# Kernel tuning notes

Measured on AMD Instinct MI355X. Metric: run time of the kernel, lower is better.

The kernel has to match this reference:

```python
import jax, jax.numpy as jnp
import numpy as np
from jax import lax

DIM = 256
WS = 8            # window side -> N = 64
H = 8             # num_heads
HD = DIM // H     # head dim = 32
NREF = 30
RB = 4            # reference batch
NWIN = 144        # windows per image (96x96 / 8x8)
N = WS * WS
B_ = RB * NWIN
SCALE = HD ** -0.5
LN_EPS = 1e-5


def make_rel_index():
    coords = np.stack(np.meshgrid(np.arange(WS), np.arange(WS), indexing='ij'))  # (2,WS,WS)
    cf = coords.reshape(2, -1)
    rel = (cf[:, :, None] - cf[:, None, :]).transpose(1, 2, 0).astype(np.int64)
    rel[..., 0] += WS - 1
    rel[..., 1] += WS - 1
    rel[..., 0] *= 2 * WS - 1
    return jnp.asarray(rel.sum(-1), jnp.int32)  # (N, N)


def setup_inputs() -> dict:
    key = jax.random.key(0)
    ks = jax.random.split(key, 10)
    return {
        'x': jax.random.normal(ks[0], (B_, N, DIM), jnp.float32),
        'mask': jnp.zeros((NWIN, N, N), jnp.float32),
        'x_ref': jax.random.normal(ks[1], (RB, DIM, NREF), jnp.float32),
        'qkv_w': jax.random.normal(ks[2], (3 * DIM, DIM), jnp.float32) * 0.02,
        'qkv_b': jnp.zeros((3 * DIM,), jnp.float32),
        'proj_w': jax.random.normal(ks[3], (DIM, DIM), jnp.float32) * 0.02,
        'proj_b': jnp.zeros((DIM,), jnp.float32),
        'bias_table': jax.random.normal(ks[4], ((2 * WS - 1) ** 2, H), jnp.float32) * 0.02,
        'diff_mu': jax.random.normal(ks[5], (1, 1, DIM), jnp.float32),
        'diff_logsigma': jax.random.normal(ks[6], (1, 1, DIM), jnp.float32) * 0.05,
        'ref_qk_w': jax.random.normal(ks[7], (2 * NREF, NREF), jnp.float32) * 0.1,
        'ref_qk_b': jnp.zeros((2 * NREF,), jnp.float32),
        'conv_w': jax.random.normal(ks[8], (H, H, 3, 3), jnp.float32) * 0.05,
        'conv_b': jnp.zeros((H,), jnp.float32),
        'rel_index': make_rel_index(),
    }


def _layer_norm_2d(a):
    # layer norm over the last two dims, no affine (F.layer_norm(x, [n_win*N, n_rf]))
    m = jnp.mean(a, axis=(-2, -1), keepdims=True)
    v = jnp.var(a, axis=(-2, -1), keepdims=True)
    return (a - m) * lax.rsqrt(v + LN_EPS)


def reference(x, mask, x_ref, qkv_w, qkv_b, proj_w, proj_b, bias_table,
              diff_mu, diff_logsigma, ref_qk_w, ref_qk_b, conv_w, conv_b, rel_index):
    # qkv projection -> (3, B_, H, N, HD)
    qkv = (x @ qkv_w.T + qkv_b).reshape(B_, N, 3, H, HD).transpose(2, 0, 3, 1, 4)
    q, k, v = qkv[0], qkv[1], qkv[2]

    # reference queries/values: x_ref (RB, DIM, NREF) -> (RB, 2*NREF, DIM)
    ref = (x_ref @ ref_qk_w.T + ref_qk_b).transpose(0, 2, 1)
    ref_q = diff_mu + jnp.exp(diff_logsigma) * ref[:, :NREF]   # (RB, NREF, DIM)
    ref_q = ref_q.reshape(RB, NREF, H, HD).transpose(0, 2, 1, 3)       # (RB, H, NREF, HD)
    ref_v = ref[:, NREF:].reshape(RB, NREF, H, HD).transpose(0, 2, 1, 3)

    # cross-attn scores q @ ref_k^T, broadcast ref over windows of the same batch
    qb = q.reshape(RB, NWIN, H, N, HD)
    ref_attn = jnp.einsum('bwhnd,bhrd->bhwnr', qb, ref_q)  # (RB, H, NWIN, N, NREF)
    ref_attn = ref_attn.reshape(RB, H, NWIN * N, NREF)

    # 3-step conv diffusion refinement with layernorm+gelu residual
    for _ in range(3):
        upd = lax.conv_general_dilated(
            ref_attn, conv_w, window_strides=(1, 1), padding=((1, 1), (1, 1)),
            dimension_numbers=('NCHW', 'OIHW', 'NCHW')) + conv_b[None, :, None, None]
        ref_attn = ref_attn + jax.nn.gelu(_layer_norm_2d(upd), approximate=False)

    ref_attn = ref_attn.reshape(RB, H, NWIN, N, NREF).transpose(0, 2, 1, 3, 4)  # (RB,NWIN,H,N,NREF)
    ref_attn = jax.nn.softmax(ref_attn, axis=-1)
    q_new = jnp.einsum('bwhnr,bhrd->bwhnd', ref_attn, ref_v) * SCALE

    # window attention with relative position bias + mask
    attn = jnp.einsum('bwhnd,bwhmd->bwhnm', q_new, k.reshape(RB, NWIN, H, N, HD))
    rel_bias = bias_table[rel_index.reshape(-1)].reshape(N, N, H).transpose(2, 0, 1)  # (H,N,N)
    attn = attn + rel_bias[None, None] + mask[None, :, None]
    attn = jax.nn.softmax(attn, axis=-1)

    out = jnp.einsum('bwhnm,bwhmd->bwhnd', attn, v.reshape(RB, NWIN, H, N, HD))
    out = out.transpose(0, 1, 3, 2, 4).reshape(B_, N, DIM)
    return out @ proj_w.T + proj_b
```

## Files before the change

### kernel.cpp

```cpp
#include <hip/hip_runtime.h>
#include <math.h>

#define NHD 8
#define HD 32
#define NREF 30
#define RB 4
#define NWIN 144
#define NTOK 64
#define IMG_H (NWIN*NTOK)
#define LN_CNT (IMG_H*NREF)
#define SCALE 0.1767766952966369f
#define LN_EPS 1e-5f

typedef __attribute__((ext_vector_type(8))) short bf8_t;
typedef __attribute__((ext_vector_type(4))) float f4_t;

__device__ __forceinline__ float gelu_f(float v) {
    return 0.5f * v * (1.0f + erff(v * 0.7071067811865476f));
}

__device__ __forceinline__ short f2bf(float f) {
    union { float f; unsigned u; } v; v.f = f;
    unsigned r = v.u + 0x7fffu + ((v.u >> 16) & 1u);
    return (short)(r >> 16);
}

__device__ __forceinline__ float bf2f(unsigned short u) {
    union { unsigned u; float f; } v; v.u = ((unsigned)u) << 16;
    return v.f;
}

__global__ __launch_bounds__(256) void k_prep(
    const float* __restrict__ x, unsigned short* __restrict__ xb,
    const float* __restrict__ qkv_w, unsigned short* __restrict__ wqb,
    const float* __restrict__ proj_w, unsigned short* __restrict__ wpb,
    const float* __restrict__ mask, const float* __restrict__ bias_table,
    const int* __restrict__ rel_index, float* __restrict__ bmt,
    const float* __restrict__ x_ref, const float* __restrict__ rw,
    const float* __restrict__ rbias, const float* __restrict__ dmu,
    const float* __restrict__ dls, float* __restrict__ ref_q,
    float* __restrict__ ref_v) {
    __shared__ float shbuf[4160 + 1800];
    const int bid = blockIdx.x;
    const int t = threadIdx.x;
    if (bid < 2048) {
        const int n8 = 9437184 / 8;
        for (int i = bid * 256 + t; i < n8; i += 2048 * 256) {
            const float* s = x + (size_t)i * 8;
            float4 a = *reinterpret_cast<const float4*>(s);
            float4 b = *reinterpret_cast<const float4*>(s + 4);
            bf8_t p;
            p[0] = f2bf(a.x); p[1] = f2bf(a.y); p[2] = f2bf(a.z); p[3] = f2bf(a.w);
            p[4] = f2bf(b.x); p[5] = f2bf(b.y); p[6] = f2bf(b.z); p[7] = f2bf(b.w);
            *reinterpret_cast<bf8_t*>(xb + (size_t)i * 8) = p;
        }
    } else if (bid < 2192) {
        const int w = bid - 2048;
        float* lm = shbuf;
        float* lb = shbuf + 4160;
        for (int u = t; u < 4096; u += 256)
            lm[(u >> 6) * 65 + (u & 63)] = mask[(size_t)w * 4096 + u];
        for (int u = t; u < 1800; u += 256) lb[u] = bias_table[u];
        __syncthreads();
        for (int u = t; u < 4096; u += 256) {
            const int m = u >> 6, n = u & 63;
            const float mv = lm[n * 65 + m];
            const int ri = rel_index[n * 64 + m];
#pragma unroll
            for (int h = 0; h < 8; ++h)
                bmt[(size_t)(w * 8 + h) * 4096 + u] = mv + lb[ri * 8 + h];
        }
    } else if (bid < 2288) {
        const int b2 = bid - 2192;
        const int n8 = 196608 / 8;
        for (int i = b2 * 256 + t; i < n8; i += 96 * 256) {
            const float* s = qkv_w + (size_t)i * 8;
            float4 a = *reinterpret_cast<const float4*>(s);
            float4 b = *reinterpret_cast<const float4*>(s + 4);
            bf8_t p;
            p[0] = f2bf(a.x); p[1] = f2bf(a.y); p[2] = f2bf(a.z); p[3] = f2bf(a.w);
            p[4] = f2bf(b.x); p[5] = f2bf(b.y); p[6] = f2bf(b.z); p[7] = f2bf(b.w);
            *reinterpret_cast<bf8_t*>(wqb + (size_t)i * 8) = p;
        }
    } else if (bid < 2320) {
        const int b2 = bid - 2288;
        const int n8 = 65536 / 8;
        for (int i = b2 * 256 + t; i < n8; i += 32 * 256) {
            const float* s = proj_w + (size_t)i * 8;
            float4 a = *reinterpret_cast<const float4*>(s);
            float4 b = *reinterpret_cast<const float4*>(s + 4);
            bf8_t p;
            p[0] = f2bf(a.x); p[1] = f2bf(a.y); p[2] = f2bf(a.z); p[3] = f2bf(a.w);
            p[4] = f2bf(b.x); p[5] = f2bf(b.y); p[6] = f2bf(b.z); p[7] = f2bf(b.w);
            *reinterpret_cast<bf8_t*>(wpb + (size_t)i * 8) = p;
        }
    } else {
        float* Wl = shbuf;
        float* Bl = shbuf + 60 * NREF;
        const int rb = bid - 2320;
        for (int i = t; i < 60 * NREF; i += 256) Wl[i] = rw[i];
        if (t < 60) Bl[t] = rbias[t];
        __syncthreads();
        const int d = t;
        float xr[NREF];
#pragma unroll
        for (int r = 0; r < NREF; ++r) xr[r] = x_ref[(rb * 256 + d) * NREF + r];
        const int h = d >> 5, hd = d & 31;
        const float mu = dmu[d], sg = expf(dls[d]);
        for (int j = 0; j < 60; ++j) {
            float acc = Bl[j];
#pragma unroll
            for (int r = 0; r < NREF; ++r) acc += xr[r] * Wl[j * NREF + r];
            if (j < NREF)
                ref_q[((rb * NHD + h) * NREF + j) * HD + hd] = mu + sg * acc;
            else
                ref_v[((rb * NHD + h) * NREF + (j - NREF)) * HD + hd] = acc;
        }
    }
}

__global__ __launch_bounds__(256) void k_qkv_mfma(
    const unsigned short* __restrict__ xb, const unsigned short* __restrict__ wb,
    const float* __restrict__ bias, unsigned short* __restrict__ qb,
    unsigned short* __restrict__ kb, unsigned short* __restrict__ vb) {
    __shared__ __align__(16) char As[128 * 128];
    __shared__ __align__(16) char Bs[128 * 128];
    const int t = threadIdx.x;
    const int bid = blockIdx.x;
    const int swz = (bid & 7) * (1728 / 8) + (bid >> 3);
    const int r0 = (swz / 6) * 128;
    const int c0 = (swz % 6) * 128;
    const int wid = t >> 6, l = t & 63;
    const int wr = wid >> 1, wc = wid & 1;
    const int lr = l & 15, lg = l >> 4;
    f4_t acc[4][4] = {};
    bf8_t ra[4], rb_[4];
#pragma unroll
    for (int i = 0; i < 4; ++i) {
        const int u = t + 256 * i;
        const int row = u >> 3, c8 = u & 7;
        ra[i]  = *reinterpret_cast<const bf8_t*>(&xb[(size_t)(r0 + row) * 256 + c8 * 8]);
        rb_[i] = *reinterpret_cast<const bf8_t*>(&wb[(size_t)(c0 + row) * 256 + c8 * 8]);
    }
#pragma unroll 1
    for (int ks = 0; ks < 4; ++ks) {
#pragma unroll
        for (int i = 0; i < 4; ++i) {
            const int u = t + 256 * i;
            const int row = u >> 3, c8 = u & 7;
            *reinterpret_cast<bf8_t*>(As + row * 128 + ((c8 * 16) ^ ((row & 7) << 4))) = ra[i];
            *reinterpret_cast<bf8_t*>(Bs + row * 128 + ((c8 * 16) ^ ((row & 7) << 4))) = rb_[i];
        }
        __syncthreads();
        if (ks < 3) {
            const int k0n = (ks + 1) * 64;
#pragma unroll
            for (int i = 0; i < 4; ++i) {
                const int u = t + 256 * i;
                const int row = u >> 3, c8 = u & 7;
                ra[i]  = *reinterpret_cast<const bf8_t*>(&xb[(size_t)(r0 + row) * 256 + k0n + c8 * 8]);
                rb_[i] = *reinterpret_cast<const bf8_t*>(&wb[(size_t)(c0 + row) * 256 + k0n + c8 * 8]);
            }
        }
#pragma unroll
        for (int kk = 0; kk < 2; ++kk) {
            bf8_t a[4], b[4];
#pragma unroll
            for (int mt = 0; mt < 4; ++mt) {
                const int row = wr * 64 + mt * 16 + lr;
                a[mt] = *reinterpret_cast<const bf8_t*>(
                    As + row * 128 + ((kk * 64 + lg * 16) ^ ((row & 7) << 4)));
            }
#pragma unroll
            for (int nt = 0; nt < 4; ++nt) {
                const int row = wc * 64 + nt * 16 + lr;
                b[nt] = *reinterpret_cast<const bf8_t*>(
                    Bs + row * 128 + ((kk * 64 + lg * 16) ^ ((row & 7) << 4)));
            }
#pragma unroll
            for (int mt = 0; mt < 4; ++mt)
#pragma unroll
                for (int nt = 0; nt < 4; ++nt)
                    acc[mt][nt] = __builtin_amdgcn_mfma_f32_16x16x32_bf16(a[mt], b[nt], acc[mt][nt], 0, 0, 0);
        }
        __syncthreads();
    }
#pragma unroll
    for (int nt = 0; nt < 4; ++nt) {
        const int gc = c0 + wc * 64 + nt * 16 + lr;
        const int i3 = gc >> 8, rem = gc & 255;
        const int h = rem >> 5, hd = rem & 31;
        const float bv = bias[gc];
        unsigned short* dst = (i3 == 0) ? qb : (i3 == 1) ? kb : vb;
#pragma unroll
        for (int mt = 0; mt < 4; ++mt)
#pragma unroll
            for (int j = 0; j < 4; ++j) {
                const int gr = r0 + wr * 64 + mt * 16 + lg * 4 + j;
                const int bb = gr >> 6, n = gr & 63;
                dst[(size_t)((bb * NHD + h) * NTOK + n) * HD + hd] =
                    (unsigned short)f2bf(acc[mt][nt][j] + bv);
            }
    }
}

__global__ __launch_bounds__(256) void k_proj_mfma(
    const unsigned short* __restrict__ A, const unsigned short* __restrict__ w,
    const float* __restrict__ bias, float* __restrict__ out) {
    __shared__ __align__(16) char As[128 * 128];
    __shared__ __align__(16) char Bs[128 * 128];
    const int t = threadIdx.x;
    const int bid = blockIdx.x;
    const int swz = (bid & 7) * (576 / 8) + (bid >> 3);
    const int r0 = (swz / 2) * 128;
    const int c0 = (swz % 2) * 128;
    const int wid = t >> 6, l = t & 63;
    const int wr = wid >> 1, wc = wid & 1;
    const int lr = l & 15, lg = l >> 4;
    f4_t acc[4][4] = {};
    bf8_t ra[4], rb_[4];
#pragma unroll
    for (int i = 0; i < 4; ++i) {
        const int u = t + 256 * i;
        const int row = u >> 3, c8 = u & 7;
        ra[i]  = *reinterpret_cast<const bf8_t*>(&A[(size_t)(r0 + row) * 256 + c8 * 8]);
        rb_[i] = *reinterpret_cast<const bf8_t*>(&w[(size_t)(c0 + row) * 256 + c8 * 8]);
    }
#pragma unroll 1
    for (int ks = 0; ks < 4; ++ks) {
#pragma unroll
        for (int i = 0; i < 4; ++i) {
            const int u = t + 256 * i;
            const int row = u >> 3, c8 = u & 7;
            *reinterpret_cast<bf8_t*>(As + row * 128 + ((c8 * 16) ^ ((row & 7) << 4))) = ra[i];
            *reinterpret_cast<bf8_t*>(Bs + row * 128 + ((c8 * 16) ^ ((row & 7) << 4))) = rb_[i];
        }
        __syncthreads();
        if (ks < 3) {
            const int k0n = (ks + 1) * 64;
#pragma unroll
            for (int i = 0; i < 4; ++i) {
                const int u = t + 256 * i;
                const int row = u >> 3, c8 = u & 7;
                ra[i]  = *reinterpret_cast<const bf8_t*>(&A[(size_t)(r0 + row) * 256 + k0n + c8 * 8]);
                rb_[i] = *reinterpret_cast<const bf8_t*>(&w[(size_t)(c0 + row) * 256 + k0n + c8 * 8]);
            }
        }
#pragma unroll
        for (int kk = 0; kk < 2; ++kk) {
            bf8_t a[4], b[4];
#pragma unroll
            for (int mt = 0; mt < 4; ++mt) {
                const int row = wr * 64 + mt * 16 + lr;
                a[mt] = *reinterpret_cast<const bf8_t*>(
                    As + row * 128 + ((kk * 64 + lg * 16) ^ ((row & 7) << 4)));
            }
#pragma unroll
            for (int nt = 0; nt < 4; ++nt) {
                const int row = wc * 64 + nt * 16 + lr;
                b[nt] = *reinterpret_cast<const bf8_t*>(
                    Bs + row * 128 + ((kk * 64 + lg * 16) ^ ((row & 7) << 4)));
            }
#pragma unroll
            for (int mt = 0; mt < 4; ++mt)
#pragma unroll
                for (int nt = 0; nt < 4; ++nt)
                    acc[mt][nt] = __builtin_amdgcn_mfma_f32_16x16x32_bf16(a[mt], b[nt], acc[mt][nt], 0, 0, 0);
        }
        __syncthreads();
    }
#pragma unroll
    for (int nt = 0; nt < 4; ++nt) {
        const int gc = c0 + wc * 64 + nt * 16 + lr;
        const float bv = bias[gc];
#pragma unroll
        for (int mt = 0; mt < 4; ++mt)
#pragma unroll
            for (int j = 0; j < 4; ++j) {
                const int gr = r0 + wr * 64 + mt * 16 + lg * 4 + j;
                out[(size_t)gr * 256 + gc] = acc[mt][nt][j] + bv;
            }
    }
}

__global__ __launch_bounds__(256) void k_scores(
    const unsigned short* __restrict__ qbuf, const float* __restrict__ ref_q,
    float* __restrict__ scores) {
    const int bid = blockIdx.x;
    const int wg = bid % 36;
    const int rh = bid / 36;
    const int h = rh % NHD, rb = rh / NHD;
    __shared__ __align__(16) float rs[NREF][32];
    __shared__ float outb[4][64 * NREF];
    const int t = threadIdx.x;
    const int wv = t >> 6, n = t & 63;
    const float* rsrc = &ref_q[(size_t)rh * NREF * HD];
    for (int u = t; u < NREF * 8; u += 256) {
        const int row = u >> 3, c4 = u & 7;
        *reinterpret_cast<float4*>(&rs[row][c4 * 4]) =
            *reinterpret_cast<const float4*>(&rsrc[u * 4]);
    }
    __syncthreads();
    const int w = wg * 4 + wv;
    const unsigned short* qsrc = &qbuf[(size_t)((rb * NWIN + w) * NHD + h) * NTOK * HD + n * 32];
    float q[32];
#pragma unroll
    for (int c8 = 0; c8 < 4; ++c8) {
        bf8_t v = *reinterpret_cast<const bf8_t*>(&qsrc[c8 * 8]);
#pragma unroll
        for (int j = 0; j < 8; ++j)
            q[c8 * 8 + j] = bf2f((unsigned short)v[j]);
    }
    for (int r = 0; r < NREF; ++r) {
        float acc = 0.f;
#pragma unroll
        for (int d = 0; d < 32; ++d) acc += q[d] * rs[r][d];
        outb[wv][n * NREF + r] = acc;
    }
    float* dst = &scores[(size_t)((rb * NHD + h) * IMG_H + w * 64) * NREF];
    for (int u = n; u < 64 * NREF; u += 64) dst[u] = outb[wv][u];
}

template<int FUSED>
__global__ __launch_bounds__(256) void k_conv_mfma(
    const float* __restrict__ scPrev, const unsigned short* __restrict__ updPrev,
    const float* __restrict__ stPrev, const float* __restrict__ conv_w,
    const float* __restrict__ conv_b, float* __restrict__ scOut,
    unsigned short* __restrict__ updOut, float* __restrict__ stats) {
    const int bid = blockIdx.x;
    const int rb = bid / 288;
    const int y0 = (bid % 288) * 32;
    __shared__ __align__(16) unsigned short At[34][32][8];
    __shared__ float red[4][8][2];
    __shared__ float lmean[8], lrsig[8];
    const int t = threadIdx.x;
    if (FUSED) {
        if (t < 8) {
            const float s0 = stPrev[(rb * NHD + t) * 2];
            const float s1 = stPrev[(rb * NHD + t) * 2 + 1];
            const float m = s0 * (1.f / LN_CNT);
            const float v = s1 * (1.f / LN_CNT) - m * m;
            lmean[t] = m;
            lrsig[t] = rsqrtf(v + LN_EPS);
        }
        __syncthreads();
    }
    for (int f = t; f < 34 * 2; f += 256) {
        const int yy = f >> 1, side = (f & 1) ? 31 : 0;
        bf8_t z;
#pragma unroll
        for (int j = 0; j < 8; ++j) z[j] = 0;
        *reinterpret_cast<bf8_t*>(&At[yy][side][0]) = z;
    }
    for (int ps = t; ps < 34 * 8 * 15; ps += 256) {
        const int yy = ps / 120;
        const int rem = ps % 120;
        const int ci = rem / 15, xh = rem % 15;
        const int xc = xh * 2;
        const int y = y0 - 1 + yy;
        unsigned short v0 = 0, v1 = 0;
        if (y >= 0 && y < IMG_H) {
            const size_t idx = (size_t)((rb * NHD + ci) * IMG_H + y) * NREF + xc;
            float2 sv = *reinterpret_cast<const float2*>(&scPrev[idx]);
            float a0, a1;
            if (FUSED) {
                const unsigned u2 = *reinterpret_cast<const unsigned*>(&updPrev[idx]);
                a0 = sv.x + gelu_f((bf2f((unsigned short)(u2 & 0xffffu)) - lmean[ci]) * lrsig[ci]);
                a1 = sv.y + gelu_f((bf2f((unsigned short)(u2 >> 16)) - lmean[ci]) * lrsig[ci]);
                if (yy >= 1 && yy <= 32) {
                    float2 so; so.x = a0; so.y = a1;
                    *reinterpret_cast<float2*>(&scOut[idx]) = so;
                }
            } else {
                a0 = sv.x; a1 = sv.y;
            }
            v0 = (unsigned short)f2bf(a0);
            v1 = (unsigned short)f2bf(a1);
        }
        At[yy][xc + 1][ci] = v0;
        At[yy][xc + 2][ci] = v1;
    }
    const int l = t & 63, wv = t >> 6;
    const int lr = l & 15, lg = l >> 4;
    bf8_t wf[3];
#pragma unroll
    for (int kg = 0; kg < 3; ++kg) {
        const int tap = kg * 4 + lg;
        bf8_t wq;
#pragma unroll
        for (int j = 0; j < 8; ++j) wq[j] = 0;
        if (lr < 8 && tap < 9) {
            const int dy = tap / 3, dx = tap % 3;
#pragma unroll
            for (int ci = 0; ci < 8; ++ci)
                wq[ci] = f2bf(conv_w[lr * 72 + ci * 9 + dy * 3 + dx]);
        }
        wf[kg] = wq;
    }
    const float cb = (lr < 8) ? conv_b[lr] : 0.f;
    __syncthreads();
    float ls = 0.f, lss = 0.f;
#pragma unroll 1
    for (int ti = 0; ti < 15; ++ti) {
        const int tile = wv * 15 + ti;
        const int pA = tile * 16 + lr;
        const int ylA = pA / 30, xA = pA % 30;
        f4_t o;
        o[0] = cb; o[1] = cb; o[2] = cb; o[3] = cb;
#pragma unroll
        for (int kg = 0; kg < 3; ++kg) {
            const int tap = kg * 4 + lg;
            const int dy = (tap < 9) ? tap / 3 : 0;
            const int dx = (tap < 9) ? tap % 3 : 0;
            bf8_t a = *reinterpret_cast<const bf8_t*>(&At[ylA + dy][xA + dx][0]);
            o = __builtin_amdgcn_mfma_f32_16x16x32_bf16(a, wf[kg], o, 0, 0, 0);
        }
        if (lr < 8) {
#pragma unroll
            for (int j = 0; j < 4; ++j) {
                const int pD = tile * 16 + lg * 4 + j;
                const int yl = pD / 30, x = pD % 30;
                updOut[(size_t)((rb * NHD + lr) * IMG_H + y0 + yl) * NREF + x] =
                    (unsigned short)f2bf(o[j]);
                ls += o[j];
                lss += o[j] * o[j];
            }
        }
    }
    ls += __shfl_xor(ls, 16); ls += __shfl_xor(ls, 32);
    lss += __shfl_xor(lss, 16); lss += __shfl_xor(lss, 32);
    if (l < 8) { red[wv][l][0] = ls; red[wv][l][1] = lss; }
    __syncthreads();
    if (t < 8) {
        atomicAdd(&stats[(rb * NHD + t) * 2],
                  red[0][t][0] + red[1][t][0] + red[2][t][0] + red[3][t][0]);
        atomicAdd(&stats[(rb * NHD + t) * 2 + 1],
                  red[0][t][1] + red[1][t][1] + red[2][t][1] + red[3][t][1]);
    }
}

__global__ __launch_bounds__(256) void k_qnewf(
    const float* __restrict__ scores, const unsigned short* __restrict__ upd,
    const float* __restrict__ st, const float* __restrict__ ref_v,
    unsigned short* __restrict__ qbuf) {
    const int bid = blockIdx.x;
    const int wg = bid % 36;
    const int rh = bid / 36;
    const int h = rh % NHD, rb = rh / NHD;
    __shared__ __align__(16) float rv[NREF][32];
    __shared__ float sl[4][64 * NREF];
    const int t = threadIdx.x;
    const int wv = t >> 6, n = t & 63;
    const float s0 = st[rh * 2], s1 = st[rh * 2 + 1];
    const float mean = s0 * (1.f / LN_CNT);
    const float var = s1 * (1.f / LN_CNT) - mean * mean;
    const float rsig = rsqrtf(var + LN_EPS);
    const float* rvs = &ref_v[(size_t)rh * NREF * HD];
    for (int u = t; u < NREF * 8; u += 256) {
        const int r = u >> 3, c4 = u & 7;
        *reinterpret_cast<float4*>(&rv[r][c4 * 4]) =
            *reinterpret_cast<const float4*>(&rvs[u * 4]);
    }
    const int w = wg * 4 + wv;
    const size_t base = (size_t)((rb * NHD + h) * IMG_H + w * 64) * NREF;
    for (int u = n; u < 64 * NREF; u += 64) {
        const float uv = bf2f(upd[base + u]);
        sl[wv][u] = scores[base + u] + gelu_f((uv - mean) * rsig);
    }
    __syncthreads();
    float p[NREF];
    float mx = -1e30f;
#pragma unroll
    for (int r = 0; r < NREF; ++r) { p[r] = sl[wv][n * NREF + r]; mx = fmaxf(mx, p[r]); }
    float sum = 0.f;
#pragma unroll
    for (int r = 0; r < NREF; ++r) { p[r] = expf(p[r] - mx); sum += p[r]; }
    const float inv = SCALE / sum;
    float acc[32] = {0.f};
#pragma unroll
    for (int r = 0; r < NREF; ++r) {
        const float pr = p[r] * inv;
#pragma unroll
        for (int d = 0; d < 32; ++d) acc[d] += pr * rv[r][d];
    }
    unsigned short* dst = &qbuf[(size_t)((rb * NWIN + w) * NHD + h) * NTOK * HD + n * 32];
#pragma unroll
    for (int c8 = 0; c8 < 4; ++c8) {
        bf8_t pk;
#pragma unroll
        for (int j = 0; j < 8; ++j) pk[j] = f2bf(acc[c8 * 8 + j]);
        *reinterpret_cast<bf8_t*>(&dst[c8 * 8]) = pk;
    }
}

__global__ __launch_bounds__(256, 4) void k_wattn_mfma(
    const unsigned short* __restrict__ qbuf, const unsigned short* __restrict__ kbuf,
    const unsigned short* __restrict__ vbuf, const float* __restrict__ bmt,
    unsigned short* __restrict__ pre) {
    const int wh = blockIdx.x;
    const int w = wh >> 3, h = wh & 7;
    const int t = threadIdx.x;
    const int rb = t >> 6;
    const int l = t & 63;
    const int lr = l & 15, lg = l >> 4;
    const int b = rb * NWIN + w;
    const int bid = b * NHD + h;
    __shared__ __align__(16) char P[4][64 * 128];

    f4_t acc[4][4];
    const float* bm = &bmt[(size_t)wh * 4096];
#pragma unroll
    for (int mt = 0; mt < 4; ++mt)
#pragma unroll
        for (int nt = 0; nt < 4; ++nt)
#pragma unroll
            for (int j = 0; j < 4; ++j)
                acc[mt][nt][j] = bm[(mt * 16 + lg * 4 + j) * 64 + nt * 16 + lr];

    const unsigned short* kp = &kbuf[(size_t)bid * 2048];
    const unsigned short* qp = &qbuf[(size_t)bid * 2048];
    bf8_t kf[4], qf[4];
#pragma unroll
    for (int mt = 0; mt < 4; ++mt) {
        kf[mt] = *reinterpret_cast<const bf8_t*>(&kp[(mt * 16 + lr) * 32 + lg * 8]);
        qf[mt] = *reinterpret_cast<const bf8_t*>(&qp[(mt * 16 + lr) * 32 + lg * 8]);
    }
#pragma unroll
    for (int mt = 0; mt < 4; ++mt)
#pragma unroll
        for (int nt = 0; nt < 4; ++nt)
            acc[mt][nt] = __builtin_amdgcn_mfma_f32_16x16x32_bf16(kf[mt], qf[nt], acc[mt][nt], 0, 0, 0);

#pragma unroll
    for (int nt = 0; nt < 4; ++nt) {
        float mx = -1e30f;
#pragma unroll
        for (int mt = 0; mt < 4; ++mt)
#pragma unroll
            for (int j = 0; j < 4; ++j) mx = fmaxf(mx, acc[mt][nt][j]);
        mx = fmaxf(mx, __shfl_xor(mx, 16));
        mx = fmaxf(mx, __shfl_xor(mx, 32));
        float s = 0.f;
#pragma unroll
        for (int mt = 0; mt < 4; ++mt)
#pragma unroll
            for (int j = 0; j < 4; ++j) {
                const float e = expf(acc[mt][nt][j] - mx);
                acc[mt][nt][j] = e;
                s += e;
            }
        s += __shfl_xor(s, 16);
        s += __shfl_xor(s, 32);
        const float inv = 1.f / s;
#pragma unroll
        for (int mt = 0; mt < 4; ++mt)
#pragma unroll
            for (int j = 0; j < 4; ++j) acc[mt][nt][j] *= inv;
    }

    const int n7 = (lr & 7) << 4;
    char* Pw = P[rb];
#pragma unroll
    for (int nt = 0; nt < 4; ++nt) {
        const int rowb = (nt * 16 + lr) * 128;
#pragma unroll
        for (int mt = 0; mt < 4; ++mt)
#pragma unroll
            for (int jp = 0; jp < 2; ++jp) {
                const unsigned lo = (unsigned short)f2bf(acc[mt][nt][jp * 2]);
                const unsigned hi = (unsigned short)f2bf(acc[mt][nt][jp * 2 + 1]);
                const int mb = (mt * 16 + lg * 4 + jp * 2) * 2;
                *reinterpret_cast<unsigned*>(&Pw[rowb + (mb ^ n7)]) = lo | (hi << 16);
            }
    }
    __syncthreads();

    const unsigned short* vp = &vbuf[(size_t)bid * 2048];
    bf8_t vf[2][2];
#pragma unroll
    for (int ht = 0; ht < 2; ++ht)
#pragma unroll
        for (int ks = 0; ks < 2; ++ks) {
            bf8_t tv;
#pragma unroll
            for (int j = 0; j < 8; ++j)
                tv[j] = (short)vp[(ks * 32 + lg * 8 + j) * 32 + ht * 16 + lr];
            vf[ht][ks] = tv;
        }

    f4_t o[2][4] = {};
#pragma unroll
    for (int ks = 0; ks < 2; ++ks)
#pragma unroll
        for (int nt = 0; nt < 4; ++nt) {
            const int rowb = (nt * 16 + lr) * 128;
            bf8_t pf = *reinterpret_cast<const bf8_t*>(&Pw[rowb + ((ks * 64 + lg * 16) ^ n7)]);
#pragma unroll
            for (int ht = 0; ht < 2; ++ht)
                o[ht][nt] = __builtin_amdgcn_mfma_f32_16x16x32_bf16(vf[ht][ks], pf, o[ht][nt], 0, 0, 0);
        }

#pragma unroll
    for (int ht = 0; ht < 2; ++ht)
#pragma unroll
        for (int nt = 0; nt < 4; ++nt) {
            ushort4 pk;
            pk.x = (unsigned short)f2bf(o[ht][nt][0]);
            pk.y = (unsigned short)f2bf(o[ht][nt][1]);
            pk.z = (unsigned short)f2bf(o[ht][nt][2]);
            pk.w = (unsigned short)f2bf(o[ht][nt][3]);
            const int n = nt * 16 + lr;
            const int hd = ht * 16 + lg * 4;
            *reinterpret_cast<ushort4*>(&pre[(size_t)(b * 64 + n) * 256 + h * 32 + hd]) = pk;
        }
}

extern "C" void kernel_launch(void* const* d_in, const int* in_sizes, int n_in,
                              void* d_out, int out_size, void* d_ws, size_t ws_size,
                              hipStream_t stream) {
    const float* x          = (const float*)d_in[0];
    const float* mask       = (const float*)d_in[1];
    const float* x_ref      = (const float*)d_in[2];
    const float* qkv_w      = (const float*)d_in[3];
    const float* qkv_b      = (const float*)d_in[4];
    const float* proj_w     = (const float*)d_in[5];
    const float* proj_b     = (const float*)d_in[6];
    const float* bias_table = (const float*)d_in[7];
    const float* diff_mu    = (const float*)d_in[8];
    const float* diff_ls    = (const float*)d_in[9];
    const float* ref_qk_w   = (const float*)d_in[10];
    const float* ref_qk_b   = (const float*)d_in[11];
    const float* conv_w     = (const float*)d_in[12];
    const float* conv_b     = (const float*)d_in[13];
    const int*   rel_index  = (const int*)d_in[14];
    float* out = (float*)d_out;

    unsigned short* xb   = (unsigned short*)d_ws;
    unsigned short* qb16 = xb + 9437184;
    unsigned short* kb16 = qb16 + 9437184;
    unsigned short* vb16 = kb16 + 9437184;
    float* scA           = (float*)(vb16 + 9437184);
    unsigned short* updA = (unsigned short*)(scA + 8847360);
    unsigned short* updB = updA + 8847360;
    float* rq            = (float*)(updB + 8847360);
    float* rv            = rq + 30720;
    float* st            = rv + 30720;
    float* bmt           = st + 192;
    unsigned short* wqb  = (unsigned short*)(bmt + 4718592);
    unsigned short* wpb  = wqb + 196608;
    float* scB           = (float*)d_ws;
    unsigned short* pre  = (unsigned short*)scA;

    k_prep<<<2324, 256, 0, stream>>>(x, xb, qkv_w, wqb, proj_w, wpb,
                                     mask, bias_table, rel_index, bmt,
                                     x_ref, ref_qk_w, ref_qk_b, diff_mu, diff_ls,
                                     rq, rv);
    k_qkv_mfma<<<1728, 256, 0, stream>>>(xb, wqb, qkv_b, qb16, kb16, vb16);
    k_scores<<<RB * NHD * 36, 256, 0, stream>>>(qb16, rq, scA);
    hipMemsetAsync(st, 0, 192 * sizeof(float), stream);
    k_conv_mfma<0><<<RB * 288, 256, 0, stream>>>(scA, updA, st, conv_w, conv_b, scB, updA, st);
    k_conv_mfma<1><<<RB * 288, 256, 0, stream>>>(scA, updA, st, conv_w, conv_b, scB, updB, st + 64);
    k_conv_mfma<1><<<RB * 288, 256, 0, stream>>>(scB, updB, st + 64, conv_w, conv_b, scA, updA, st + 128);
    k_qnewf<<<RB * NHD * 36, 256, 0, stream>>>(scA, updA, st + 128, rv, qb16);
    k_wattn_mfma<<<NWIN * NHD, 256, 0, stream>>>(qb16, kb16, vb16, bmt, pre);
    k_proj_mfma<<<576, 256, 0, stream>>>(pre, wpb, proj_b, out);
}
```

Measured before the change: 259.7 us.

## Store score/update buffers channel-last to vectorize conv staging

Changes the intermediate score and conv-update buffers from a head-major (rb,h,y,x) layout to a channel-last (rb,y,x,h) layout, so each conv staging thread loads all 8 heads of a pixel with wide float4/bf16x8 loads and writes one packed LDS vector. k_scores and k_qnewf are reorganized to one block per window covering all heads, with thread h=t&7 so stores and loads interleave heads. This removes scalar 2-element strided gathers and per-element LDS writes in the three conv passes. The trade-off is that per-thread accesses in scores/qnewf become stride-8 and the rs/rv tables grow to cover all heads in LDS.

```diff
diff --git a/kernel.cpp b/kernel.cpp
--- a/kernel.cpp
+++ b/kernel.cpp
@@ -287,38 +287,35 @@
     const unsigned short* __restrict__ qbuf, const float* __restrict__ ref_q,
     float* __restrict__ scores) {
     const int bid = blockIdx.x;
-    const int wg = bid % 36;
-    const int rh = bid / 36;
-    const int h = rh % NHD, rb = rh / NHD;
-    __shared__ __align__(16) float rs[NREF][32];
-    __shared__ float outb[4][64 * NREF];
+    const int w = bid % NWIN, rb = bid / NWIN;
+    __shared__ __align__(16) float rs[8][NREF][32];
     const int t = threadIdx.x;
-    const int wv = t >> 6, n = t & 63;
-    const float* rsrc = &ref_q[(size_t)rh * NREF * HD];
-    for (int u = t; u < NREF * 8; u += 256) {
-        const int row = u >> 3, c4 = u & 7;
-        *reinterpret_cast<float4*>(&rs[row][c4 * 4]) =
-            *reinterpret_cast<const float4*>(&rsrc[u * 4]);
-    }
+    for (int u = t; u < 1920; u += 256)
+        *reinterpret_cast<float4*>(&rs[0][0][0] + u * 4) =
+            *reinterpret_cast<const float4*>(&ref_q[(size_t)rb * 7680 + u * 4]);
     __syncthreads();
-    const int w = wg * 4 + wv;
-    const unsigned short* qsrc = &qbuf[(size_t)((rb * NWIN + w) * NHD + h) * NTOK * HD + n * 32];
-    float q[32];
-#pragma unroll
-    for (int c8 = 0; c8 < 4; ++c8) {
-        bf8_t v = *reinterpret_cast<const bf8_t*>(&qsrc[c8 * 8]);
-#pragma unroll
-        for (int j = 0; j < 8; ++j)
-            q[c8 * 8 + j] = bf2f((unsigned short)v[j]);
-    }
-    for (int r = 0; r < NREF; ++r) {
-        float acc = 0.f;
-#pragma unroll
-        for (int d = 0; d < 32; ++d) acc += q[d] * rs[r][d];
-        outb[wv][n * NREF + r] = acc;
-    }
-    float* dst = &scores[(size_t)((rb * NHD + h) * IMG_H + w * 64) * NREF];
-    for (int u = n; u < 64 * NREF; u += 64) dst[u] = outb[wv][u];
+    const int h = t & 7, nb = t >> 3;
+#pragma unroll 1
+    for (int half = 0; half < 2; ++half) {
+        const int n = half * 32 + nb;
+        const unsigned short* qsrc =
+            &qbuf[(size_t)(((rb * NWIN + w) * NHD) + h) * 2048 + n * 32];
+        float q[32];
+#pragma unroll
+        for (int c8 = 0; c8 < 4; ++c8) {
+            bf8_t v = *reinterpret_cast<const bf8_t*>(&qsrc[c8 * 8]);
+#pragma unroll
+            for (int j = 0; j < 8; ++j)
+                q[c8 * 8 + j] = bf2f((unsigned short)v[j]);
+        }
+        float* dst = &scores[((size_t)(rb * IMG_H + w * 64 + n) * NREF) * NHD + h];
+        for (int r = 0; r < NREF; ++r) {
+            float acc = 0.f;
+#pragma unroll
+            for (int d = 0; d < 32; ++d) acc += q[d] * rs[h][r][d];
+            dst[r * NHD] = acc;
+        }
+    }
 }
 
 template<int FUSED>
@@ -352,33 +349,34 @@
         for (int j = 0; j < 8; ++j) z[j] = 0;
         *reinterpret_cast<bf8_t*>(&At[yy][side][0]) = z;
     }
-    for (int ps = t; ps < 34 * 8 * 15; ps += 256) {
-        const int yy = ps / 120;
-        const int rem = ps % 120;
-        const int ci = rem / 15, xh = rem % 15;
-        const int xc = xh * 2;
+    for (int ps = t; ps < 34 * 30; ps += 256) {
+        const int yy = ps / 30, xc = ps % 30;
         const int y = y0 - 1 + yy;
-        unsigned short v0 = 0, v1 = 0;
+        bf8_t pk;
+#pragma unroll
+        for (int j = 0; j < 8; ++j) pk[j] = 0;
         if (y >= 0 && y < IMG_H) {
-            const size_t idx = (size_t)((rb * NHD + ci) * IMG_H + y) * NREF + xc;
-            float2 sv = *reinterpret_cast<const float2*>(&scPrev[idx]);
-            float a0, a1;
+            const size_t idx = ((size_t)(rb * IMG_H + y) * NREF + xc) * NHD;
+            float4 s0 = *reinterpret_cast<const float4*>(&scPrev[idx]);
+            float4 s1 = *reinterpret_cast<const float4*>(&scPrev[idx + 4]);
+            float a[8] = {s0.x, s0.y, s0.z, s0.w, s1.x, s1.y, s1.z, s1.w};
             if (FUSED) {
-                const unsigned u2 = *reinterpret_cast<const unsigned*>(&updPrev[idx]);
-                a0 = sv.x + gelu_f((bf2f((unsigned short)(u2 & 0xffffu)) - lmean[ci]) * lrsig[ci]);
-                a1 = sv.y + gelu_f((bf2f((unsigned short)(u2 >> 16)) - lmean[ci]) * lrsig[ci]);
+                bf8_t u8 = *reinterpret_cast<const bf8_t*>(&updPrev[idx]);
+#pragma unroll
+                for (int ci = 0; ci < 8; ++ci)
+                    a[ci] += gelu_f((bf2f((unsigned short)u8[ci]) - lmean[ci]) * lrsig[ci]);
                 if (yy >= 1 && yy <= 32) {
-                    float2 so; so.x = a0; so.y = a1;
-                    *reinterpret_cast<float2*>(&scOut[idx]) = so;
+                    float4 o0, o1;
+                    o0.x = a[0]; o0.y = a[1]; o0.z = a[2]; o0.w = a[3];
+                    o1.x = a[4]; o1.y = a[5]; o1.z = a[6]; o1.w = a[7];
+                    *reinterpret_cast<float4*>(&scOut[idx]) = o0;
+                    *reinterpret_cast<float4*>(&scOut[idx + 4]) = o1;
                 }
-            } else {
-                a0 = sv.x; a1 = sv.y;
-            }
-            v0 = (unsigned short)f2bf(a0);
-            v1 = (unsigned short)f2bf(a1);
-        }
-        At[yy][xc + 1][ci] = v0;
-        At[yy][xc + 2][ci] = v1;
+            }
+#pragma unroll
+            for (int ci = 0; ci < 8; ++ci) pk[ci] = f2bf(a[ci]);
+        }
+        *reinterpret_cast<bf8_t*>(&At[yy][xc + 1][0]) = pk;
     }
     const int l = t & 63, wv = t >> 6;
     const int lr = l & 15, lg = l >> 4;
@@ -420,7 +418,7 @@
             for (int j = 0; j < 4; ++j) {
                 const int pD = tile * 16 + lg * 4 + j;
                 const int yl = pD / 30, x = pD % 30;
-                updOut[(size_t)((rb * NHD + lr) * IMG_H + y0 + yl) * NREF + x] =
+                updOut[((size_t)(rb * IMG_H + y0 + yl) * NREF + x) * NHD + lr] =
                     (unsigned short)f2bf(o[j]);
                 ls += o[j];
                 lss += o[j] * o[j];
@@ -444,52 +442,54 @@
     const float* __restrict__ st, const float* __restrict__ ref_v,
     unsigned short* __restrict__ qbuf) {
     const int bid = blockIdx.x;
-    const int wg = bid % 36;
-    const int rh = bid / 36;
-    const int h = rh % NHD, rb = rh / NHD;
-    __shared__ __align__(16) float rv[NREF][32];
-    __shared__ float sl[4][64 * NREF];
+    const int w = bid % NWIN, rb = bid / NWIN;
+    __shared__ __align__(16) float rv[8][NREF][32];
+    __shared__ float lmean[8], lrsig[8];
     const int t = threadIdx.x;
-    const int wv = t >> 6, n = t & 63;
-    const float s0 = st[rh * 2], s1 = st[rh * 2 + 1];
-    const float mean = s0 * (1.f / LN_CNT);
-    const float var = s1 * (1.f / LN_CNT) - mean * mean;
-    const float rsig = rsqrtf(var + LN_EPS);
-    const float* rvs = &ref_v[(size_t)rh * NREF * HD];
-    for (int u = t; u < NREF * 8; u += 256) {
-        const int r = u >> 3, c4 = u & 7;
-        *reinterpret_cast<float4*>(&rv[r][c4 * 4]) =
-            *reinterpret_cast<const float4*>(&rvs[u * 4]);
-    }
-    const int w = wg * 4 + wv;
-    const size_t base = (size_t)((rb * NHD + h) * IMG_H + w * 64) * NREF;
-    for (int u = n; u < 64 * NREF; u += 64) {
-        const float uv = bf2f(upd[base + u]);
-        sl[wv][u] = scores[base + u] + gelu_f((uv - mean) * rsig);
-    }
+    if (t < 8) {
+        const float s0 = st[(rb * NHD + t) * 2];
+        const float s1 = st[(rb * NHD + t) * 2 + 1];
+        const float m = s0 * (1.f / LN_CNT);
+        const float v = s1 * (1.f / LN_CNT) - m * m;
+        lmean[t] = m;
+        lrsig[t] = rsqrtf(v + LN_EPS);
+    }
+    for (int u = t; u < 1920; u += 256)
+        *reinterpret_cast<float4*>(&rv[0][0][0] + u * 4) =
+            *reinterpret_cast<const float4*>(&ref_v[(size_t)rb * 7680 + u * 4]);
     __syncthreads();
-    float p[NREF];
-    float mx = -1e30f;
-#pragma unroll
-    for (int r = 0; r < NREF; ++r) { p[r] = sl[wv][n * NREF + r]; mx = fmaxf(mx, p[r]); }
-    float sum = 0.f;
-#pragma unroll
-    for (int r = 0; r < NREF; ++r) { p[r] = expf(p[r] - mx); sum += p[r]; }
-    const float inv = SCALE / sum;
-    float acc[32] = {0.f};
-#pragma unroll
-    for (int r = 0; r < NREF; ++r) {
-        const float pr = p[r] * inv;
-#pragma unroll
-        for (int d = 0; d < 32; ++d) acc[d] += pr * rv[r][d];
-    }
-    unsigned short* dst = &qbuf[(size_t)((rb * NWIN + w) * NHD + h) * NTOK * HD + n * 32];
-#pragma unroll
-    for (int c8 = 0; c8 < 4; ++c8) {
-        bf8_t pk;
-#pragma unroll
-        for (int j = 0; j < 8; ++j) pk[j] = f2bf(acc[c8 * 8 + j]);
-        *reinterpret_cast<bf8_t*>(&dst[c8 * 8]) = pk;
+    const int h = t & 7, nb = t >> 3;
+#pragma unroll 1
+    for (int half = 0; half < 2; ++half) {
+        const int n = half * 32 + nb;
+        const size_t base = ((size_t)(rb * IMG_H + w * 64 + n) * NREF) * NHD + h;
+        float p[NREF];
+        float mx = -1e30f;
+        for (int r = 0; r < NREF; ++r) {
+            const float uv = bf2f(upd[base + r * NHD]);
+            p[r] = scores[base + r * NHD] + gelu_f((uv - lmean[h]) * lrsig[h]);
+            mx = fmaxf(mx, p[r]);
+        }
+        float sum = 0.f;
+#pragma unroll
+        for (int r = 0; r < NREF; ++r) { p[r] = expf(p[r] - mx); sum += p[r]; }
+        const float inv = SCALE / sum;
+        float acc[32] = {0.f};
+#pragma unroll
+        for (int r = 0; r < NREF; ++r) {
+            const float pr = p[r] * inv;
+#pragma unroll
+            for (int d = 0; d < 32; ++d) acc[d] += pr * rv[h][r][d];
+        }
+        unsigned short* dst =
+            &qbuf[(size_t)(((rb * NWIN + w) * NHD) + h) * 2048 + n * 32];
+#pragma unroll
+        for (int c8 = 0; c8 < 4; ++c8) {
+            bf8_t pk;
+#pragma unroll
+            for (int j = 0; j < 8; ++j) pk[j] = f2bf(acc[c8 * 8 + j]);
+            *reinterpret_cast<bf8_t*>(&dst[c8 * 8]) = pk;
+        }
     }
 }
 
@@ -656,12 +656,12 @@
                                      x_ref, ref_qk_w, ref_qk_b, diff_mu, diff_ls,
                                      rq, rv);
     k_qkv_mfma<<<1728, 256, 0, stream>>>(xb, wqb, qkv_b, qb16, kb16, vb16);
-    k_scores<<<RB * NHD * 36, 256, 0, stream>>>(qb16, rq, scA);
+    k_scores<<<RB * NWIN, 256, 0, stream>>>(qb16, rq, scA);
     hipMemsetAsync(st, 0, 192 * sizeof(float), stream);
     k_conv_mfma<0><<<RB * 288, 256, 0, stream>>>(scA, updA, st, conv_w, conv_b, scB, updA, st);
     k_conv_mfma<1><<<RB * 288, 256, 0, stream>>>(scA, updA, st, conv_w, conv_b, scB, updB, st + 64);
     k_conv_mfma<1><<<RB * 288, 256, 0, stream>>>(scB, updB, st + 64, conv_w, conv_b, scA, updA, st + 128);
-    k_qnewf<<<RB * NHD * 36, 256, 0, stream>>>(scA, updA, st + 128, rv, qb16);
+    k_qnewf<<<RB * NWIN, 256, 0, stream>>>(scA, updA, st + 128, rv, qb16);
     k_wattn_mfma<<<NWIN * NHD, 256, 0, stream>>>(qb16, kb16, vb16, bmt, pre);
     k_proj_mfma<<<576, 256, 0, stream>>>(pre, wpb, proj_b, out);
 }
```

After: 446.6 us. 1.72x slower.
